# Optimization experiments

Hardware: AMD Instinct MI355X
Metric: run time of the kernel (lower is better)

Reference implementation:

```python
import jax, jax.numpy as jnp
import numpy as np

BETA = 0.9  # leaky-integrator decay of the stateful neuron


def setup_inputs() -> dict:
    key = jax.random.key(0)
    k = jax.random.split(key, 5)
    B, T, I, H, O = 128, 512, 1024, 2048, 512
    x = jax.random.normal(k[0], (B, T, I), dtype=jnp.float32)
    # Linear params, PyTorch-style scaling
    W_in = jax.random.normal(k[1], (I, H), dtype=jnp.float32) / np.sqrt(I)
    b_in = jax.random.normal(k[2], (H,), dtype=jnp.float32) / np.sqrt(I)
    W_out = jax.random.normal(k[3], (H, O), dtype=jnp.float32) / np.sqrt(H)
    b_out = jax.random.normal(k[4], (O,), dtype=jnp.float32) / np.sqrt(H)
    return {"x": x, "W_in": W_in, "b_in": b_in, "W_out": W_out, "b_out": b_out}


def reference(x, W_in, b_in, W_out, b_out):
    # x: [B, T, I]
    B, T, _ = x.shape
    # fc_in applied to every timestep at once (same math as per-step Linear)
    h = jnp.einsum('bti,ih->bth', x, W_in) + b_in  # [B, T, H]

    # stateful neuron: leaky integration s_t = BETA * s_{t-1} + h_t, via scan
    def step(s, h_t):
        s = BETA * s + h_t
        return s, s

    s0 = jnp.zeros((B, h.shape[-1]), dtype=h.dtype)
    _, S = jax.lax.scan(step, s0, jnp.swapaxes(h, 0, 1))  # S: [T, B, H]

    # readout per timestep, then reduce over time (readout_mode='sum')
    logits = jnp.einsum('tbh,ho->tbo', S, W_out) + b_out  # [T, B, O]
    return logits.sum(axis=0)  # [B, O]
```

## Files before the change

### kernel.cpp

```cpp
#include <hip/hip_runtime.h>
#include <hip/hip_bf16.h>
#include <math.h>

constexpr int B_ = 128, T_ = 512, I_ = 1024, H_ = 2048, O_ = 512;
#define BETA 0.9f

constexpr int WOFF = 0;
constexpr int YOFF = 512;
constexpr int ZOFF = YOFF + B_ * I_;
constexpr int WS_FLOATS = ZOFF + B_ * H_;

typedef __attribute__((ext_vector_type(4))) short short4v;
typedef __attribute__((ext_vector_type(8))) short short8v;
typedef __attribute__((ext_vector_type(4))) float float4v;

__global__ __launch_bounds__(256) void init_kernel(float* __restrict__ ws,
                                                   const float* __restrict__ b_in,
                                                   const float* __restrict__ b_out,
                                                   float* __restrict__ out, float wsum) {
    int idx = blockIdx.x * 256 + threadIdx.x;
    const int total = WS_FLOATS + B_ * O_;
    if (idx >= total) return;
    if (idx < 512) {
        ws[idx] = (1.0f - powf(BETA, (float)(T_ - idx))) * (1.0f / (1.0f - BETA));
    } else if (idx < ZOFF) {
        ws[idx] = 0.0f;
    } else if (idx < WS_FLOATS) {
        int j = idx - ZOFF;
        ws[idx] = wsum * b_in[j & (H_ - 1)];
    } else {
        int j = idx - WS_FLOATS;
        out[j] = (float)T_ * b_out[j & (O_ - 1)];
    }
}

constexpr int TCH = 128;
__global__ __launch_bounds__(256) void wreduce_kernel(const float* __restrict__ x,
                                                      float* __restrict__ ws) {
    __shared__ float wl[TCH];
    const int b  = blockIdx.x >> 2;
    const int tc = blockIdx.x & 3;
    const int t0 = tc * TCH;
    if (threadIdx.x < TCH) wl[threadIdx.x] = ws[WOFF + t0 + threadIdx.x];
    __syncthreads();

    const int i = threadIdx.x * 4;
    const float* xp = x + (size_t)b * T_ * I_ + (size_t)t0 * I_ + i;
    float4v acc = {0.f, 0.f, 0.f, 0.f};
#pragma unroll 4
    for (int tb = 0; tb < TCH; tb += 8) {
        float4v v[8];
#pragma unroll
        for (int j = 0; j < 8; ++j)
            v[j] = *(const float4v*)(xp + (size_t)(tb + j) * I_);
#pragma unroll
        for (int j = 0; j < 8; ++j) {
            const float wt = wl[tb + j];
            acc.x += wt * v[j].x; acc.y += wt * v[j].y;
            acc.z += wt * v[j].z; acc.w += wt * v[j].w;
        }
    }
    float* yp = ws + YOFF + b * I_ + i;
    atomicAdd(yp + 0, acc.x);
    atomicAdd(yp + 1, acc.y);
    atomicAdd(yp + 2, acc.z);
    atomicAdd(yp + 3, acc.w);
}

template <int KGLOB, int NGLOB, int KCH>
__global__ __launch_bounds__(256) void mm128(const float* __restrict__ A,
                                             const float* __restrict__ Bm,
                                             float* __restrict__ C) {
    constexpr int BN = 64, BK = 32, PAD = 8;
    __shared__ __align__(16) __hip_bfloat16 As[128][BK + PAD];
    __shared__ __align__(16) __hip_bfloat16 Bs[BN][BK + PAD];

    const int n0    = blockIdx.x * BN;
    const int kbase = blockIdx.y * KCH;
    const int tid   = threadIdx.x;
    const int lane  = tid & 63;
    const int w     = tid >> 6;
    const int lo    = lane & 15;
    const int hi    = lane >> 4;

    float4v acc[2][4];
#pragma unroll
    for (int mf = 0; mf < 2; ++mf)
#pragma unroll
        for (int nf = 0; nf < 4; ++nf) acc[mf][nf] = (float4v){0.f, 0.f, 0.f, 0.f};

    for (int k0 = kbase; k0 < kbase + KCH; k0 += BK) {
        {
            const int row = tid >> 1;
            const int kh  = (tid & 1) * 16;
            const float* ap = A + (size_t)row * KGLOB + k0 + kh;
#pragma unroll
            for (int j = 0; j < 4; ++j) {
                float4 v = *(const float4*)(ap + 4 * j);
                union { short4v s; __hip_bfloat16 h[4]; } u;
                u.h[0] = __float2bfloat16(v.x); u.h[1] = __float2bfloat16(v.y);
                u.h[2] = __float2bfloat16(v.z); u.h[3] = __float2bfloat16(v.w);
                *(short4v*)&As[row][kh + 4 * j] = u.s;
            }
        }
        {
            const int k  = tid >> 3;
            const int nq = (tid & 7) * 8;
            const float* bp = Bm + (size_t)(k0 + k) * NGLOB + n0 + nq;
#pragma unroll
            for (int j = 0; j < 2; ++j) {
                float4 v = *(const float4*)(bp + 4 * j);
                Bs[nq + 4 * j + 0][k] = __float2bfloat16(v.x);
                Bs[nq + 4 * j + 1][k] = __float2bfloat16(v.y);
                Bs[nq + 4 * j + 2][k] = __float2bfloat16(v.z);
                Bs[nq + 4 * j + 3][k] = __float2bfloat16(v.w);
            }
        }
        __syncthreads();
        {
            const int kk = hi * 8;
            short8v a[2], bv[4];
#pragma unroll
            for (int mf = 0; mf < 2; ++mf)
                a[mf] = *(const short8v*)&As[w * 32 + mf * 16 + lo][kk];
#pragma unroll
            for (int nf = 0; nf < 4; ++nf)
                bv[nf] = *(const short8v*)&Bs[nf * 16 + lo][kk];
#pragma unroll
            for (int mf = 0; mf < 2; ++mf)
#pragma unroll
                for (int nf = 0; nf < 4; ++nf)
                    acc[mf][nf] = __builtin_amdgcn_mfma_f32_16x16x32_bf16(
                        a[mf], bv[nf], acc[mf][nf], 0, 0, 0);
        }
        __syncthreads();
    }
#pragma unroll
    for (int mf = 0; mf < 2; ++mf)
#pragma unroll
        for (int nf = 0; nf < 4; ++nf)
#pragma unroll
            for (int i = 0; i < 4; ++i) {
                const int row = w * 32 + mf * 16 + hi * 4 + i;
                const int col = n0 + nf * 16 + lo;
                atomicAdd(&C[(size_t)row * NGLOB + col], acc[mf][nf][i]);
            }
}

extern "C" void kernel_launch(void* const* d_in, const int* in_sizes, int n_in,
                              void* d_out, int out_size, void* d_ws, size_t ws_size,
                              hipStream_t stream) {
    const float* x     = (const float*)d_in[0];
    const float* W_in  = (const float*)d_in[1];
    const float* b_in  = (const float*)d_in[2];
    const float* W_out = (const float*)d_in[3];
    const float* b_out = (const float*)d_in[4];
    float* out = (float*)d_out;
    float* ws  = (float*)d_ws;

    const double beta = 0.9;
    const double bT = pow(beta, (double)T_);
    const float wsum = (float)(((double)T_ - beta * (1.0 - bT) / (1.0 - beta)) / (1.0 - beta));

    const int total = WS_FLOATS + B_ * O_;
    init_kernel<<<(total + 255) / 256, 256, 0, stream>>>(ws, b_in, b_out, out, wsum);

    wreduce_kernel<<<B_ * (T_ / TCH), 256, 0, stream>>>(x, ws);

    mm128<I_, H_, 128><<<dim3(H_ / 64, I_ / 128), 256, 0, stream>>>(ws + YOFF, W_in, ws + ZOFF);

    mm128<H_, O_, 64><<<dim3(O_ / 64, H_ / 64), 256, 0, stream>>>(ws + ZOFF, W_out, out);
}
```

Before: 73.64 us.

## Pretranspose weights to bf16 in init kernel and widen matmul K tile

The init kernel now also converts W_in and W_out to bf16 and transposes them into a workspace buffer. The matmul kernels then load the B operand as contiguous 16-byte vectors instead of doing scattered per-element transposed shared-memory stores. K-tile size doubles to 64 with two MFMA substeps per tile, and a manual round-to-nearest bf16 conversion replaces the library one. The transpose runs on every call and adds a pass over both weight matrices plus extra workspace, in exchange for cheaper and better-coalesced B loads.

After: 75.73 us. 1.03x slower.

```diff
diff --git a/kernel.cpp b/kernel.cpp
--- a/kernel.cpp
+++ b/kernel.cpp
@@ -5,32 +5,73 @@
 constexpr int B_ = 128, T_ = 512, I_ = 1024, H_ = 2048, O_ = 512;
 #define BETA 0.9f
 
-constexpr int WOFF = 0;
-constexpr int YOFF = 512;
-constexpr int ZOFF = YOFF + B_ * I_;
-constexpr int WS_FLOATS = ZOFF + B_ * H_;
+constexpr int WOFF  = 0;
+constexpr int YOFF  = 512;
+constexpr int ZOFF  = YOFF + B_ * I_;
+constexpr int WTI_F = ZOFF + B_ * H_;
+constexpr int WTO_F = WTI_F + (H_ * I_) / 2;
 
 typedef __attribute__((ext_vector_type(4))) short short4v;
 typedef __attribute__((ext_vector_type(8))) short short8v;
 typedef __attribute__((ext_vector_type(4))) float float4v;
 
+__device__ inline ushort f2bf(float f) {
+    union { float f; unsigned u; } c; c.f = f;
+    return (ushort)((c.u + 0x7FFF + ((c.u >> 16) & 1)) >> 16);
+}
+
+constexpr int INIT_BASE = (512 + B_ * I_ + B_ * H_ + B_ * O_ + 255) / 256;
+constexpr int TI_TILES  = (I_ / 64) * (H_ / 64);
+constexpr int TO_TILES  = (H_ / 64) * (O_ / 64);
+
+__device__ inline void transpose_tile(const float* __restrict__ src,
+                                      ushort* __restrict__ dst,
+                                      int K, int N, int tk, int tn,
+                                      ushort (*tile)[72], int tid) {
+    const int k0 = tk * 64, n0 = tn * 64;
+#pragma unroll
+    for (int rep = 0; rep < 4; ++rep) {
+        const int kr = rep * 16 + (tid >> 4);
+        const int nc = (tid & 15) * 4;
+        float4v v = *(const float4v*)(src + (size_t)(k0 + kr) * N + n0 + nc);
+        tile[nc + 0][kr] = f2bf(v.x);
+        tile[nc + 1][kr] = f2bf(v.y);
+        tile[nc + 2][kr] = f2bf(v.z);
+        tile[nc + 3][kr] = f2bf(v.w);
+    }
+    __syncthreads();
+    const int nr = tid >> 2, kc = (tid & 3) * 16;
+    ushort* dp = dst + (size_t)(n0 + nr) * K + k0 + kc;
+    *(short8v*)dp       = *(const short8v*)&tile[nr][kc];
+    *(short8v*)(dp + 8) = *(const short8v*)&tile[nr][kc + 8];
+}
+
 __global__ __launch_bounds__(256) void init_kernel(float* __restrict__ ws,
                                                    const float* __restrict__ b_in,
                                                    const float* __restrict__ b_out,
-                                                   float* __restrict__ out, float wsum) {
-    int idx = blockIdx.x * 256 + threadIdx.x;
-    const int total = WS_FLOATS + B_ * O_;
-    if (idx >= total) return;
-    if (idx < 512) {
-        ws[idx] = (1.0f - powf(BETA, (float)(T_ - idx))) * (1.0f / (1.0f - BETA));
-    } else if (idx < ZOFF) {
-        ws[idx] = 0.0f;
-    } else if (idx < WS_FLOATS) {
-        int j = idx - ZOFF;
-        ws[idx] = wsum * b_in[j & (H_ - 1)];
+                                                   float* __restrict__ out, float wsum,
+                                                   const float* __restrict__ Wi,
+                                                   const float* __restrict__ Wo) {
+    __shared__ __align__(16) ushort tile[64][72];
+    const int bid = blockIdx.x, tid = threadIdx.x;
+    if (bid < INIT_BASE) {
+        const int idx = bid * 256 + tid;
+        if (idx < 512) {
+            ws[idx] = (1.0f - powf(BETA, (float)(T_ - idx))) * (1.0f / (1.0f - BETA));
+        } else if (idx < ZOFF) {
+            ws[idx] = 0.0f;
+        } else if (idx < WTI_F) {
+            ws[idx] = wsum * b_in[(idx - ZOFF) & (H_ - 1)];
+        } else {
+            const int j = idx - WTI_F;
+            if (j < B_ * O_) out[j] = (float)T_ * b_out[j & (O_ - 1)];
+        }
+    } else if (bid < INIT_BASE + TI_TILES) {
+        const int id = bid - INIT_BASE;
+        transpose_tile(Wi, (ushort*)(ws + WTI_F), I_, H_, id >> 5, id & 31, tile, tid);
     } else {
-        int j = idx - WS_FLOATS;
-        out[j] = (float)T_ * b_out[j & (O_ - 1)];
+        const int id = bid - INIT_BASE - TI_TILES;
+        transpose_tile(Wo, (ushort*)(ws + WTO_F), H_, O_, id >> 3, id & 7, tile, tid);
     }
 }
 
@@ -68,12 +109,12 @@
 }
 
 template <int KGLOB, int NGLOB, int KCH>
-__global__ __launch_bounds__(256) void mm128(const float* __restrict__ A,
-                                             const float* __restrict__ Bm,
-                                             float* __restrict__ C) {
-    constexpr int BN = 64, BK = 32, PAD = 8;
-    __shared__ __align__(16) __hip_bfloat16 As[128][BK + PAD];
-    __shared__ __align__(16) __hip_bfloat16 Bs[BN][BK + PAD];
+__global__ __launch_bounds__(256) void mm128T(const float* __restrict__ A,
+                                              const ushort* __restrict__ Wt,
+                                              float* __restrict__ C) {
+    constexpr int BN = 64, BK = 64, PAD = 8;
+    __shared__ __align__(16) ushort As[128][BK + PAD];
+    __shared__ __align__(16) ushort Bs[BN][BK + PAD];
 
     const int n0    = blockIdx.x * BN;
     const int kbase = blockIdx.y * KCH;
@@ -92,33 +133,28 @@
     for (int k0 = kbase; k0 < kbase + KCH; k0 += BK) {
         {
             const int row = tid >> 1;
-            const int kh  = (tid & 1) * 16;
+            const int kh  = (tid & 1) * 32;
             const float* ap = A + (size_t)row * KGLOB + k0 + kh;
 #pragma unroll
-            for (int j = 0; j < 4; ++j) {
-                float4 v = *(const float4*)(ap + 4 * j);
-                union { short4v s; __hip_bfloat16 h[4]; } u;
-                u.h[0] = __float2bfloat16(v.x); u.h[1] = __float2bfloat16(v.y);
-                u.h[2] = __float2bfloat16(v.z); u.h[3] = __float2bfloat16(v.w);
-                *(short4v*)&As[row][kh + 4 * j] = u.s;
+            for (int j = 0; j < 8; ++j) {
+                float4v v = *(const float4v*)(ap + 4 * j);
+                short4v s;
+                s[0] = (short)f2bf(v.x); s[1] = (short)f2bf(v.y);
+                s[2] = (short)f2bf(v.z); s[3] = (short)f2bf(v.w);
+                *(short4v*)&As[row][kh + 4 * j] = s;
             }
         }
         {
-            const int k  = tid >> 3;
-            const int nq = (tid & 7) * 8;
-            const float* bp = Bm + (size_t)(k0 + k) * NGLOB + n0 + nq;
-#pragma unroll
-            for (int j = 0; j < 2; ++j) {
-                float4 v = *(const float4*)(bp + 4 * j);
-                Bs[nq + 4 * j + 0][k] = __float2bfloat16(v.x);
-                Bs[nq + 4 * j + 1][k] = __float2bfloat16(v.y);
-                Bs[nq + 4 * j + 2][k] = __float2bfloat16(v.z);
-                Bs[nq + 4 * j + 3][k] = __float2bfloat16(v.w);
-            }
+            const int n  = tid >> 2;
+            const int kq = (tid & 3) * 16;
+            const ushort* wp = Wt + (size_t)(n0 + n) * KGLOB + k0 + kq;
+            *(short8v*)&Bs[n][kq]     = *(const short8v*)wp;
+            *(short8v*)&Bs[n][kq + 8] = *(const short8v*)(wp + 8);
         }
         __syncthreads();
-        {
-            const int kk = hi * 8;
+#pragma unroll
+        for (int ks = 0; ks < 2; ++ks) {
+            const int kk = ks * 32 + hi * 8;
             short8v a[2], bv[4];
 #pragma unroll
             for (int mf = 0; mf < 2; ++mf)
@@ -162,12 +198,14 @@
     const double bT = pow(beta, (double)T_);
     const float wsum = (float)(((double)T_ - beta * (1.0 - bT) / (1.0 - beta)) / (1.0 - beta));
 
-    const int total = WS_FLOATS + B_ * O_;
-    init_kernel<<<(total + 255) / 256, 256, 0, stream>>>(ws, b_in, b_out, out, wsum);
+    init_kernel<<<INIT_BASE + TI_TILES + TO_TILES, 256, 0, stream>>>(
+        ws, b_in, b_out, out, wsum, W_in, W_out);
 
     wreduce_kernel<<<B_ * (T_ / TCH), 256, 0, stream>>>(x, ws);
 
-    mm128<I_, H_, 128><<<dim3(H_ / 64, I_ / 128), 256, 0, stream>>>(ws + YOFF, W_in, ws + ZOFF);
-
-    mm128<H_, O_, 64><<<dim3(O_ / 64, H_ / 64), 256, 0, stream>>>(ws + ZOFF, W_out, out);
-}
+    mm128T<I_, H_, 128><<<dim3(H_ / 64, I_ / 128), 256, 0, stream>>>(
+        ws + YOFF, (const ushort*)(ws + WTI_F), ws + ZOFF);
+
+    mm128T<H_, O_, 64><<<dim3(O_ / 64, H_ / 64), 256, 0, stream>>>(
+        ws + ZOFF, (const ushort*)(ws + WTO_F), out);
+}
```
